# Kernel tuning notes

Hardware: AMD Instinct MI355X
Metric: run time of the kernel (lower is better)

Reference implementation:

```python
import jax, jax.numpy as jnp
import numpy as np

B, T, D_IN, H = 4, 4096, 1024, 64


def setup_inputs() -> dict:
    key = jax.random.key(0)
    kx, kq, kk, kv, kbq, kbk, kbv = jax.random.split(key, 7)
    s = 0.02
    return {
        "examples": jax.random.normal(kx, (B, T, D_IN), dtype=jnp.float32),
        "Wq": jax.random.normal(kq, (H, D_IN), dtype=jnp.float32) * s,
        "bq": jax.random.normal(kbq, (H,), dtype=jnp.float32) * s,
        "Wk": jax.random.normal(kk, (H, D_IN), dtype=jnp.float32) * s,
        "bk": jax.random.normal(kbk, (H,), dtype=jnp.float32) * s,
        "Wv": jax.random.normal(kv, (H, D_IN), dtype=jnp.float32) * s,
        "bv": jax.random.normal(kbv, (H,), dtype=jnp.float32) * s,
    }


def reference(examples, Wq, bq, Wk, bk, Wv, bv):
    # Linear projections (torch Linear: x @ W.T + b)
    q = jnp.einsum('btd,hd->bth', examples, Wq) + bq  # [B,T,H]
    k = jnp.einsum('btd,hd->bth', examples, Wk) + bk
    v = jnp.einsum('btd,hd->bth', examples, Wv) + bv
    # Faithful to source: affinity = K @ Q^T (rows=key pos i, cols=query pos j),
    # no 1/sqrt(d) scaling.
    aff = jnp.einsum('bih,bjh->bij', k, q)  # [B,T,T]
    Tlen = examples.shape[1]
    mask = jnp.tril(jnp.ones((Tlen, Tlen), dtype=bool))
    aff = jnp.where(mask, aff, -jnp.inf)
    attn = jax.nn.softmax(aff, axis=-1)
    return jnp.einsum('bij,bjh->bih', attn, v)  # [B,T,H]
```

## Files before the change

kernel.cpp:

```cpp
#include <hip/hip_runtime.h>
#include <hip/hip_bf16.h>

#define BB 4
#define TT 4096
#define NTOK (BB * TT)
#define DD 1024
#define HH 64
#define NTASKS 2048

typedef __attribute__((ext_vector_type(8))) __bf16 bf16x8;
typedef __attribute__((ext_vector_type(8))) unsigned short ushort8;
typedef __attribute__((ext_vector_type(4))) float f32x4;
typedef __attribute__((ext_vector_type(4))) float f4;
typedef unsigned short u16;
typedef unsigned int u32;

__device__ __forceinline__ u16 f2bf(float f) {
  unsigned u = __builtin_bit_cast(unsigned, f);
  u += 0x7FFFu + ((u >> 16) & 1u);
  return (u16)(u >> 16);
}
__device__ __forceinline__ float bf2f(u16 s) {
  unsigned u = ((unsigned)s) << 16;
  return __builtin_bit_cast(float, u);
}
__device__ __forceinline__ f32x4 mfma16(bf16x8 a, bf16x8 b, f32x4 c) {
  return __builtin_amdgcn_mfma_f32_16x16x32_bf16(a, b, c, 0, 0, 0);
}
__device__ __forceinline__ u32 cvtpk(float lo, float hi) {
  u32 r;
  asm("v_cvt_pk_bf16_f32 %0, %1, %2" : "=v"(r) : "v"(lo), "v"(hi));
  return r;
}
__device__ __forceinline__ u32 permhi(u32 u1, u32 u0) {
  return __builtin_amdgcn_perm(u1, u0, 0x07060302u);
}
__device__ __forceinline__ void gl_lds16(const u16* g, u16* l) {
  __builtin_amdgcn_global_load_lds(
      (const __attribute__((address_space(1))) u32*)(const void*)g,
      (__attribute__((address_space(3))) u32*)(void*)l, 16, 0, 0);
}

__global__ __launch_bounds__(256) void prep_w(
    const float* __restrict__ Wq, const float* __restrict__ Wk,
    const float* __restrict__ Wv, u16* __restrict__ wpre)
{
  const int c = blockIdx.x * 256 + threadIdx.x;
  const int arr = c >> 13;
  const int rem = c & 8191;
  const int lane = rem & 63;
  const int nt = (rem >> 6) & 3;
  const int ksub = (rem >> 8) & 1;
  const int kt = rem >> 9;
  const float* W = (arr <= 1) ? Wq : (arr <= 3) ? Wk : Wv;
  const bool lo = (arr == 1) || (arr == 3);
  const int n = nt * 16 + (lane & 15);
  const int k0 = kt * 64 + ksub * 32 + (lane >> 4) * 8;
  const float* src = W + (size_t)n * DD + k0;
  ushort8 out;
#pragma unroll
  for (int e = 0; e < 8; ++e) {
    const float f = src[e];
    const u16 h = f2bf(f);
    out[e] = lo ? f2bf(f - bf2f(h)) : h;
  }
  *(ushort8*)(wpre + (size_t)arr * 65536 + (size_t)rem * 8) = out;
}

__global__ __launch_bounds__(256) void proj_kernel(
    const float* __restrict__ x,
    const float* __restrict__ bq, const float* __restrict__ bk,
    const float* __restrict__ bv, const u16* __restrict__ wpre,
    u16* __restrict__ qhi, u16* __restrict__ qlo,
    u16* __restrict__ khi, u16* __restrict__ klo,
    u16* __restrict__ vt)
{
  const int tid = threadIdx.x;
  const int w = tid >> 6;
  const int lane = tid & 63;
  const int l15 = lane & 15;
  const int g4 = lane >> 4;
  const int rb = blockIdx.x & 255;
  const int type = blockIdx.x >> 8;
  const bool isv = (type == 2);
  const u16* whiP = wpre + (size_t)((type == 0) ? 0 : (type == 1) ? 2 : 4) * 65536;
  const int mrow = rb * 64 + w * 16 + l15;
  const float* xrow = x + (size_t)mrow * DD;

  f32x4 acc[4];
#pragma unroll
  for (int i = 0; i < 4; ++i) acc[i] = (f32x4){0.f, 0.f, 0.f, 0.f};

  for (int kt = 0; kt < 16; ++kt) {
#pragma unroll
    for (int ksub = 0; ksub < 2; ++ksub) {
      const float* xs = xrow + kt * 64 + ksub * 32 + g4 * 8;
      const f4 a = *(const f4*)xs;
      const f4 b2 = *(const f4*)(xs + 4);
      u32 xh32[4], xl32[4];
#pragma unroll
      for (int p = 0; p < 4; ++p) {
        const float f0 = (p < 2) ? a[2 * p] : b2[2 * p - 4];
        const float f1 = (p < 2) ? a[2 * p + 1] : b2[2 * p - 3];
        const u32 u0 = __builtin_bit_cast(u32, f0);
        const u32 u1 = __builtin_bit_cast(u32, f1);
        xh32[p] = permhi(u1, u0);
        const float h0 = __builtin_bit_cast(float, u0 & 0xFFFF0000u);
        const float h1 = __builtin_bit_cast(float, u1 & 0xFFFF0000u);
        const u32 v0 = __builtin_bit_cast(u32, f0 - h0);
        const u32 v1 = __builtin_bit_cast(u32, f1 - h1);
        xl32[p] = permhi(v1, v0);
      }
      bf16x8 xh, xl;
#pragma unroll
      for (int p = 0; p < 4; ++p) {
        ((u32*)&xh)[p] = xh32[p];
        ((u32*)&xl)[p] = xl32[p];
      }
      const u16* fb = whiP + ((kt * 2 + ksub) * 4) * 512 + lane * 8;
#pragma unroll
      for (int nt = 0; nt < 4; ++nt) {
        const bf16x8 bhi = *(const bf16x8*)(fb + nt * 512);
        acc[nt] = mfma16(xh, bhi, acc[nt]);
        if (!isv) {
          const bf16x8 blo = *(const bf16x8*)(fb + 65536 + nt * 512);
          acc[nt] = mfma16(xh, blo, acc[nt]);
          acc[nt] = mfma16(xl, bhi, acc[nt]);
        }
      }
    }
  }
  const float* bias = (type == 0) ? bq : (type == 1) ? bk : bv;
#pragma unroll
  for (int nt = 0; nt < 4; ++nt) {
    const int col = nt * 16 + l15;
    const float bb = bias[col];
#pragma unroll
    for (int rr = 0; rr < 4; ++rr) {
      const int row = rb * 64 + w * 16 + g4 * 4 + rr;
      const float val = acc[nt][rr] + bb;
      const u16 h = f2bf(val);
      if (type < 2) {
        const int colS = ((((col >> 3) ^ (row & 7)) << 3) | (col & 7));
        u16* hiP = (type == 0) ? qhi : khi;
        u16* loP = (type == 0) ? qlo : klo;
        hiP[(size_t)row * HH + colS] = h;
        loP[(size_t)row * HH + colS] = f2bf(val - bf2f(h));
      } else {
        vt[(size_t)col * NTOK + row] = h;
      }
    }
  }
}

__global__ __launch_bounds__(256) void attn_kernel(
    const u16* __restrict__ qhi, const u16* __restrict__ qlo,
    const u16* __restrict__ khi, const u16* __restrict__ klo,
    const u16* __restrict__ vt, u16* __restrict__ Opart,
    float* __restrict__ ml)
{
  __shared__ __attribute__((aligned(16))) u16 qh_lds[2][64][64];
  __shared__ __attribute__((aligned(16))) u16 ql_lds[2][64][64];
  __shared__ __attribute__((aligned(16))) u16 plds[4][16][72];
  const int tid = threadIdx.x;
  const int lane = tid & 63;
  const int w = tid >> 6;
  const int l15 = lane & 15;
  const int g4 = lane >> 4;

  const int b = blockIdx.x >> 9;
  const int TW = (blockIdx.x >> 3) & 63;
  const int s = blockIdx.x & 7;
  const int ns = (TW + 8) >> 3;
  if (s >= ns) return;
  const int jt0 = s * 8;
  const int jt1 = (jt0 + 8 < TW + 1) ? jt0 + 8 : TW + 1;
  const int rowbase = TW * 64 + w * 16;

  bf16x8 kh[2], kl[2];
#pragma unroll
  for (int ksub = 0; ksub < 2; ++ksub) {
    const size_t ro = (size_t)(b * TT + rowbase + l15) * HH;
    const int ch = ((ksub * 4 + g4) ^ (l15 & 7)) * 8;
    kh[ksub] = *(const bf16x8*)(khi + ro + ch);
    kl[ksub] = *(const bf16x8*)(klo + ro + ch);
  }

  auto stage = [&](int buf, int jt) {
    const size_t gbase = (size_t)(b * TT + jt * 64) * HH;
    const int rsrc = (lane >> 3);
    const int csrc = (lane & 7) * 8;
#pragma unroll
    for (int i = 0; i < 2; ++i) {
      const int r0 = w * 16 + i * 8;
      const size_t src = gbase + (size_t)(r0 + rsrc) * HH + csrc;
      gl_lds16(qhi + src, &qh_lds[buf][r0][0]);
      gl_lds16(qlo + src, &ql_lds[buf][r0][0]);
    }
  };

  float m = -INFINITY, lsum = 0.f;
  f32x4 O[4];
#pragma unroll
  for (int ht = 0; ht < 4; ++ht) O[ht] = (f32x4){0.f, 0.f, 0.f, 0.f};

  stage(0, jt0);
  __syncthreads();
  int cur = 0;
  for (int jt = jt0; jt < jt1; ++jt) {
    if (jt + 1 < jt1) stage(cur ^ 1, jt + 1);
    f32x4 S[4];
#pragma unroll
    for (int nt = 0; nt < 4; ++nt) S[nt] = (f32x4){0.f, 0.f, 0.f, 0.f};
#pragma unroll
    for (int nt = 0; nt < 4; ++nt) {
      const int row = nt * 16 + l15;
      const int c0 = (g4 ^ (l15 & 7)) * 8;
      const int c1 = ((4 + g4) ^ (l15 & 7)) * 8;
      const bf16x8 q0 = *(const bf16x8*)&qh_lds[cur][row][c0];
      const bf16x8 q1 = *(const bf16x8*)&qh_lds[cur][row][c1];
      const bf16x8 ql0 = *(const bf16x8*)&ql_lds[cur][row][c0];
      const bf16x8 ql1 = *(const bf16x8*)&ql_lds[cur][row][c1];
      S[nt] = mfma16(q0, kh[0], S[nt]);
      S[nt] = mfma16(q1, kh[1], S[nt]);
      S[nt] = mfma16(ql0, kh[0], S[nt]);
      S[nt] = mfma16(ql1, kh[1], S[nt]);
      S[nt] = mfma16(q0, kl[0], S[nt]);
      S[nt] = mfma16(q1, kl[1], S[nt]);
    }
    if (jt == TW) {
      const int ii = rowbase + l15;
#pragma unroll
      for (int nt = 0; nt < 4; ++nt)
#pragma unroll
        for (int rr = 0; rr < 4; ++rr) {
          const int jj = jt * 64 + nt * 16 + g4 * 4 + rr;
          if (jj > ii) S[nt][rr] = -INFINITY;
        }
    }
    float tm = -INFINITY;
#pragma unroll
    for (int nt = 0; nt < 4; ++nt)
#pragma unroll
      for (int rr = 0; rr < 4; ++rr) tm = fmaxf(tm, S[nt][rr]);
    tm = fmaxf(tm, __shfl_xor(tm, 16));
    tm = fmaxf(tm, __shfl_xor(tm, 32));
    const float mnew = fmaxf(m, tm);
    const float sc = __expf(m - mnew);
    m = mnew;
    float ssum = 0.f;
#pragma unroll
    for (int nt = 0; nt < 4; ++nt)
#pragma unroll
      for (int rr = 0; rr < 4; ++rr) {
        const float p = __expf(S[nt][rr] - mnew);
        S[nt][rr] = p;
        ssum += p;
      }
    ssum += __shfl_xor(ssum, 16);
    ssum += __shfl_xor(ssum, 32);
    lsum = lsum * sc + ssum;
#pragma unroll
    for (int ht = 0; ht < 4; ++ht)
#pragma unroll
      for (int rr = 0; rr < 4; ++rr) O[ht][rr] *= sc;
#pragma unroll
    for (int nt = 0; nt < 4; ++nt) {
      *(u32*)&plds[w][l15][nt * 16 + g4 * 4] = cvtpk(S[nt][0], S[nt][1]);
      *(u32*)&plds[w][l15][nt * 16 + g4 * 4 + 2] = cvtpk(S[nt][2], S[nt][3]);
    }
    const int j0 = jt * 64;
#pragma unroll
    for (int kt2 = 0; kt2 < 2; ++kt2) {
      const bf16x8 pf = *(const bf16x8*)&plds[w][l15][kt2 * 32 + g4 * 8];
#pragma unroll
      for (int ht = 0; ht < 4; ++ht) {
        const u16* vp = vt + (size_t)(ht * 16 + l15) * NTOK + b * TT + j0 +
                        kt2 * 32 + g4 * 8;
        O[ht] = mfma16(*(const bf16x8*)vp, pf, O[ht]);
      }
    }
    __syncthreads();
    cur ^= 1;
  }
  const int task = blockIdx.x;
  u16* opb = Opart + (size_t)task * 4096;
#pragma unroll
  for (int ht = 0; ht < 4; ++ht)
#pragma unroll
    for (int rr = 0; rr < 4; ++rr)
      opb[(ht * 16 + g4 * 4 + rr) * 64 + w * 16 + l15] = f2bf(O[ht][rr]);
  if (g4 == 0) {
    ml[task * 64 + w * 16 + l15] = m;
    ml[NTASKS * 64 + task * 64 + w * 16 + l15] = lsum;
  }
}

__global__ __launch_bounds__(256) void combine_kernel(
    const u16* __restrict__ Opart, const float* __restrict__ ml,
    float* __restrict__ out)
{
  __shared__ float lt[64][65];
  const int tid = threadIdx.x;
  const int b = blockIdx.x >> 6;
  const int TW = blockIdx.x & 63;
  const int ns = (TW + 8) >> 3;
  const int tb = blockIdx.x * 8;
  const int ro = tid & 63;
  const int hq = tid >> 6;
  const float* mb = ml;
  const float* lb = ml + NTASKS * 64;

  float M = -INFINITY;
  for (int ss = 0; ss < ns; ++ss)
    M = fmaxf(M, mb[(tb + ss) * 64 + ro]);
  float L = 0.f;
  float acc[16];
#pragma unroll
  for (int hh = 0; hh < 16; ++hh) acc[hh] = 0.f;
  for (int ss = 0; ss < ns; ++ss) {
    const float e = __expf(mb[(tb + ss) * 64 + ro] - M);
    L += e * lb[(tb + ss) * 64 + ro];
    const u16* op = Opart + (size_t)(tb + ss) * 4096 + hq * 16 * 64 + ro;
#pragma unroll
    for (int hh = 0; hh < 16; ++hh) acc[hh] += e * bf2f(op[hh * 64]);
  }
  const float rL = 1.f / L;
#pragma unroll
  for (int hh = 0; hh < 16; ++hh) lt[ro][hq * 16 + hh] = acc[hh] * rL;
  __syncthreads();
  const int h2 = tid & 63;
  const int rq = tid >> 6;
#pragma unroll
  for (int pp = 0; pp < 16; ++pp) {
    const int r = rq * 16 + pp;
    out[(size_t)(b * TT + TW * 64 + r) * HH + h2] = lt[r][h2];
  }
}

extern "C" void kernel_launch(void* const* d_in, const int* in_sizes, int n_in,
                              void* d_out, int out_size, void* d_ws, size_t ws_size,
                              hipStream_t stream) {
  (void)in_sizes; (void)n_in; (void)out_size; (void)ws_size;
  const float* x  = (const float*)d_in[0];
  const float* Wq = (const float*)d_in[1];
  const float* bq = (const float*)d_in[2];
  const float* Wk = (const float*)d_in[3];
  const float* bk = (const float*)d_in[4];
  const float* Wv = (const float*)d_in[5];
  const float* bv = (const float*)d_in[6];
  float* out = (float*)d_out;

  u16* ws   = (u16*)d_ws;
  u16* wpre = ws;
  u16* qhi  = ws + 5 * 65536;
  u16* qlo  = qhi + (size_t)NTOK * HH;
  u16* khi  = qlo + (size_t)NTOK * HH;
  u16* klo  = khi + (size_t)NTOK * HH;
  u16* vt   = klo + (size_t)NTOK * HH;
  u16* Opart = vt + (size_t)NTOK * HH;
  float* ml  = (float*)(Opart + (size_t)NTASKS * 4096);

  prep_w<<<160, 256, 0, stream>>>(Wq, Wk, Wv, wpre);
  proj_kernel<<<768, 256, 0, stream>>>(x, bq, bk, bv, wpre,
                                       qhi, qlo, khi, klo, vt);
  attn_kernel<<<NTASKS, 256, 0, stream>>>(qhi, qlo, khi, klo, vt, Opart, ml);
  combine_kernel<<<256, 256, 0, stream>>>(Opart, ml, out);
}
```

Baseline: 273.1 us.

## Software-pipeline projection loads, prefetch V fragments, and widen combine grid

```diff
diff --git a/kernel.cpp b/kernel.cpp
--- a/kernel.cpp
+++ b/kernel.cpp
@@ -67,7 +67,7 @@
   *(ushort8*)(wpre + (size_t)arr * 65536 + (size_t)rem * 8) = out;
 }
 
-__global__ __launch_bounds__(256) void proj_kernel(
+__global__ __launch_bounds__(256, 3) void proj_kernel(
     const float* __restrict__ x,
     const float* __restrict__ bq, const float* __restrict__ bk,
     const float* __restrict__ bv, const u16* __restrict__ wpre,
@@ -91,45 +91,64 @@
 #pragma unroll
   for (int i = 0; i < 4; ++i) acc[i] = (f32x4){0.f, 0.f, 0.f, 0.f};
 
-  for (int kt = 0; kt < 16; ++kt) {
-#pragma unroll
-    for (int ksub = 0; ksub < 2; ++ksub) {
-      const float* xs = xrow + kt * 64 + ksub * 32 + g4 * 8;
-      const f4 a = *(const f4*)xs;
-      const f4 b2 = *(const f4*)(xs + 4);
-      u32 xh32[4], xl32[4];
-#pragma unroll
-      for (int p = 0; p < 4; ++p) {
-        const float f0 = (p < 2) ? a[2 * p] : b2[2 * p - 4];
-        const float f1 = (p < 2) ? a[2 * p + 1] : b2[2 * p - 3];
-        const u32 u0 = __builtin_bit_cast(u32, f0);
-        const u32 u1 = __builtin_bit_cast(u32, f1);
-        xh32[p] = permhi(u1, u0);
-        const float h0 = __builtin_bit_cast(float, u0 & 0xFFFF0000u);
-        const float h1 = __builtin_bit_cast(float, u1 & 0xFFFF0000u);
-        const u32 v0 = __builtin_bit_cast(u32, f0 - h0);
-        const u32 v1 = __builtin_bit_cast(u32, f1 - h1);
-        xl32[p] = permhi(v1, v0);
-      }
-      bf16x8 xh, xl;
-#pragma unroll
-      for (int p = 0; p < 4; ++p) {
-        ((u32*)&xh)[p] = xh32[p];
-        ((u32*)&xl)[p] = xl32[p];
-      }
-      const u16* fb = whiP + ((kt * 2 + ksub) * 4) * 512 + lane * 8;
-#pragma unroll
-      for (int nt = 0; nt < 4; ++nt) {
-        const bf16x8 bhi = *(const bf16x8*)(fb + nt * 512);
-        acc[nt] = mfma16(xh, bhi, acc[nt]);
-        if (!isv) {
-          const bf16x8 blo = *(const bf16x8*)(fb + 65536 + nt * 512);
-          acc[nt] = mfma16(xh, blo, acc[nt]);
-          acc[nt] = mfma16(xl, bhi, acc[nt]);
-        }
-      }
-    }
-  }
+  f4 xaA, xbA, xaB, xbB;
+  bf16x8 whA[4], wlA[4], whB[4], wlB[4];
+
+#define LOAD_ITER(XA, XB, WH, WL, IT)                                         \
+  {                                                                           \
+    const float* xs_ = xrow + (IT) * 32 + g4 * 8;                             \
+    XA = *(const f4*)xs_;                                                     \
+    XB = *(const f4*)(xs_ + 4);                                               \
+    const u16* fb_ = whiP + (IT) * 2048 + lane * 8;                           \
+    _Pragma("unroll")                                                         \
+    for (int nt_ = 0; nt_ < 4; ++nt_) {                                       \
+      WH[nt_] = *(const bf16x8*)(fb_ + nt_ * 512);                            \
+      if (!isv) WL[nt_] = *(const bf16x8*)(fb_ + 65536 + nt_ * 512);          \
+    }                                                                         \
+  }
+
+#define MFMA_ITER(XA, XB, WH, WL)                                             \
+  {                                                                           \
+    u32 xh32_[4], xl32_[4];                                                   \
+    _Pragma("unroll")                                                         \
+    for (int p_ = 0; p_ < 4; ++p_) {                                          \
+      const float f0_ = (p_ < 2) ? XA[2 * p_] : XB[2 * p_ - 4];               \
+      const float f1_ = (p_ < 2) ? XA[2 * p_ + 1] : XB[2 * p_ - 3];           \
+      const u32 u0_ = __builtin_bit_cast(u32, f0_);                           \
+      const u32 u1_ = __builtin_bit_cast(u32, f1_);                           \
+      xh32_[p_] = permhi(u1_, u0_);                                           \
+      const float h0_ = __builtin_bit_cast(float, u0_ & 0xFFFF0000u);         \
+      const float h1_ = __builtin_bit_cast(float, u1_ & 0xFFFF0000u);         \
+      xl32_[p_] = permhi(__builtin_bit_cast(u32, f1_ - h1_),                  \
+                         __builtin_bit_cast(u32, f0_ - h0_));                 \
+    }                                                                         \
+    bf16x8 xh_, xl_;                                                          \
+    _Pragma("unroll")                                                         \
+    for (int p_ = 0; p_ < 4; ++p_) {                                          \
+      ((u32*)&xh_)[p_] = xh32_[p_];                                           \
+      ((u32*)&xl_)[p_] = xl32_[p_];                                           \
+    }                                                                         \
+    _Pragma("unroll")                                                         \
+    for (int nt_ = 0; nt_ < 4; ++nt_) {                                       \
+      acc[nt_] = mfma16(xh_, WH[nt_], acc[nt_]);                              \
+      if (!isv) {                                                             \
+        acc[nt_] = mfma16(xh_, WL[nt_], acc[nt_]);                            \
+        acc[nt_] = mfma16(xl_, WH[nt_], acc[nt_]);                            \
+      }                                                                       \
+    }                                                                         \
+  }
+
+  LOAD_ITER(xaA, xbA, whA, wlA, 0)
+#pragma unroll
+  for (int it2 = 0; it2 < 16; ++it2) {
+    LOAD_ITER(xaB, xbB, whB, wlB, 2 * it2 + 1)
+    MFMA_ITER(xaA, xbA, whA, wlA)
+    if (it2 < 15) LOAD_ITER(xaA, xbA, whA, wlA, 2 * it2 + 2)
+    MFMA_ITER(xaB, xbB, whB, wlB)
+  }
+#undef LOAD_ITER
+#undef MFMA_ITER
+
   const float* bias = (type == 0) ? bq : (type == 1) ? bk : bv;
 #pragma unroll
   for (int nt = 0; nt < 4; ++nt) {
@@ -209,6 +228,14 @@
   int cur = 0;
   for (int jt = jt0; jt < jt1; ++jt) {
     if (jt + 1 < jt1) stage(cur ^ 1, jt + 1);
+    const int j0 = jt * 64;
+    bf16x8 vf[8];
+#pragma unroll
+    for (int kt2 = 0; kt2 < 2; ++kt2)
+#pragma unroll
+      for (int ht = 0; ht < 4; ++ht)
+        vf[kt2 * 4 + ht] = *(const bf16x8*)(vt + (size_t)(ht * 16 + l15) * NTOK +
+                                            b * TT + j0 + kt2 * 32 + g4 * 8);
     f32x4 S[4];
 #pragma unroll
     for (int nt = 0; nt < 4; ++nt) S[nt] = (f32x4){0.f, 0.f, 0.f, 0.f};
@@ -269,16 +296,12 @@
       *(u32*)&plds[w][l15][nt * 16 + g4 * 4] = cvtpk(S[nt][0], S[nt][1]);
       *(u32*)&plds[w][l15][nt * 16 + g4 * 4 + 2] = cvtpk(S[nt][2], S[nt][3]);
     }
-    const int j0 = jt * 64;
 #pragma unroll
     for (int kt2 = 0; kt2 < 2; ++kt2) {
       const bf16x8 pf = *(const bf16x8*)&plds[w][l15][kt2 * 32 + g4 * 8];
 #pragma unroll
-      for (int ht = 0; ht < 4; ++ht) {
-        const u16* vp = vt + (size_t)(ht * 16 + l15) * NTOK + b * TT + j0 +
-                        kt2 * 32 + g4 * 8;
-        O[ht] = mfma16(*(const bf16x8*)vp, pf, O[ht]);
-      }
+      for (int ht = 0; ht < 4; ++ht)
+        O[ht] = mfma16(vf[kt2 * 4 + ht], pf, O[ht]);
     }
     __syncthreads();
     cur ^= 1;
@@ -300,14 +323,16 @@
     const u16* __restrict__ Opart, const float* __restrict__ ml,
     float* __restrict__ out)
 {
-  __shared__ float lt[64][65];
+  __shared__ float lt[64][17];
   const int tid = threadIdx.x;
-  const int b = blockIdx.x >> 6;
-  const int TW = blockIdx.x & 63;
+  const int b = blockIdx.x >> 8;
+  const int rem = blockIdx.x & 255;
+  const int TW = rem >> 2;
+  const int hq = rem & 3;
   const int ns = (TW + 8) >> 3;
-  const int tb = blockIdx.x * 8;
+  const int tb = ((b << 6) | TW) * 8;
   const int ro = tid & 63;
-  const int hq = tid >> 6;
+  const int hh4 = tid >> 6;
   const float* mb = ml;
   const float* lb = ml + NTASKS * 64;
 
@@ -315,26 +340,25 @@
   for (int ss = 0; ss < ns; ++ss)
     M = fmaxf(M, mb[(tb + ss) * 64 + ro]);
   float L = 0.f;
-  float acc[16];
-#pragma unroll
-  for (int hh = 0; hh < 16; ++hh) acc[hh] = 0.f;
+  float acc[4] = {0.f, 0.f, 0.f, 0.f};
   for (int ss = 0; ss < ns; ++ss) {
     const float e = __expf(mb[(tb + ss) * 64 + ro] - M);
     L += e * lb[(tb + ss) * 64 + ro];
-    const u16* op = Opart + (size_t)(tb + ss) * 4096 + hq * 16 * 64 + ro;
-#pragma unroll
-    for (int hh = 0; hh < 16; ++hh) acc[hh] += e * bf2f(op[hh * 64]);
+    const u16* op = Opart + (size_t)(tb + ss) * 4096 +
+                    (hq * 16 + hh4 * 4) * 64 + ro;
+#pragma unroll
+    for (int et = 0; et < 4; ++et) acc[et] += e * bf2f(op[et * 64]);
   }
   const float rL = 1.f / L;
 #pragma unroll
-  for (int hh = 0; hh < 16; ++hh) lt[ro][hq * 16 + hh] = acc[hh] * rL;
+  for (int et = 0; et < 4; ++et) lt[ro][hh4 * 4 + et] = acc[et] * rL;
   __syncthreads();
-  const int h2 = tid & 63;
-  const int rq = tid >> 6;
-#pragma unroll
-  for (int pp = 0; pp < 16; ++pp) {
-    const int r = rq * 16 + pp;
-    out[(size_t)(b * TT + TW * 64 + r) * HH + h2] = lt[r][h2];
+  const int hh = tid & 15;
+  const int rq = tid >> 4;
+#pragma unroll
+  for (int pp = 0; pp < 4; ++pp) {
+    const int r = pp * 16 + rq;
+    out[(size_t)(b * TT + TW * 64 + r) * HH + hq * 16 + hh] = lt[r][hh];
   }
 }
 
@@ -365,5 +389,5 @@
   proj_kernel<<<768, 256, 0, stream>>>(x, bq, bk, bv, wpre,
                                        qhi, qlo, khi, klo, vt);
   attn_kernel<<<NTASKS, 256, 0, stream>>>(qhi, qlo, khi, klo, vt, Opart, ml);
-  combine_kernel<<<256, 256, 0, stream>>>(Opart, ml, out);
-}
+  combine_kernel<<<1024, 256, 0, stream>>>(Opart, ml, out);
+}
```

After: 235.8 us. 1.16x faster.
